# Optimization experiments

Hardware: AMD Instinct MI355X
Metric: run time of the kernel (lower is better)

## Reference

```python
import jax, jax.numpy as jnp
import numpy as np

E = 1024
H = 16
D = E // H
NUM_BUCKETS = 320
MAX_DISTANCE = 800


def _relative_positions_bucket(relative_positions):
    # relative_positions: int32 [T, S]
    num_buckets = NUM_BUCKETS // 2  # 160
    relative_buckets = (relative_positions > 0).astype(jnp.int32) * num_buckets
    rel = jnp.abs(relative_positions)
    max_exact = num_buckets // 2  # 80
    is_small = rel < max_exact
    rel_f = jnp.maximum(rel, 1).astype(jnp.float32)
    large = jnp.log(rel_f / max_exact) / np.log(MAX_DISTANCE / max_exact) * (num_buckets - max_exact)
    large = (max_exact + large).astype(jnp.int32)
    large = jnp.minimum(large, num_buckets - 1)
    relative_buckets = relative_buckets + jnp.where(is_small, rel, large)
    return relative_buckets


def setup_inputs() -> dict:
    key = jax.random.key(0)
    ks = jax.random.split(key, 12)
    B, T = 2, 2048
    s = 0.02
    return {
        "hidden_states": jax.random.normal(ks[0], (B, T, E), dtype=jnp.float32),
        "q_w": jax.random.normal(ks[1], (E, E), dtype=jnp.float32) * s,
        "q_b": jnp.zeros((E,), dtype=jnp.float32),
        "k_w": jax.random.normal(ks[2], (E, E), dtype=jnp.float32) * s,
        "k_b": jnp.zeros((E,), dtype=jnp.float32),
        "v_w": jax.random.normal(ks[3], (E, E), dtype=jnp.float32) * s,
        "v_b": jnp.zeros((E,), dtype=jnp.float32),
        "out_w": jax.random.normal(ks[4], (E, E), dtype=jnp.float32) * s,
        "out_b": jnp.zeros((E,), dtype=jnp.float32),
        "rel_embed": jax.random.normal(ks[5], (NUM_BUCKETS, H), dtype=jnp.float32) * s,
        "gru_const": jnp.ones((1, H, 1, 1), dtype=jnp.float32),
        "gru_w": jax.random.normal(ks[6], (8, D), dtype=jnp.float32) * s,
        "gru_b": jnp.zeros((8,), dtype=jnp.float32),
    }


def reference(hidden_states, q_w, q_b, k_w, k_b, v_w, v_b, out_w, out_b,
              rel_embed, gru_const, gru_w, gru_b):
    B, T, _ = hidden_states.shape
    scaling = D ** (-0.5)

    # --- relative position bias: [H, T, T] ---
    ctx = jnp.arange(T, dtype=jnp.int32)[:, None]
    mem = jnp.arange(T, dtype=jnp.int32)[None, :]
    buckets = _relative_positions_bucket(mem - ctx)          # [T, T]
    position_bias = rel_embed[buckets]                        # [T, T, H]
    position_bias = jnp.transpose(position_bias, (2, 0, 1))   # [H, T, T]

    # --- gate (gru_rel_pos): per (b, h, t) scalar ---
    gated = hidden_states.reshape(B, T, H, D).transpose(0, 2, 1, 3)  # [B,H,T,D]
    proj = jnp.einsum('bhtd,ed->bhte', gated, gru_w) + gru_b         # [B,H,T,8]
    proj = proj.reshape(B, H, T, 2, 4).sum(-1)                        # [B,H,T,2]
    gate = jax.nn.sigmoid(proj)
    gate_a = gate[..., 0:1]
    gate_b = gate[..., 1:2]
    gate_out = gate_a * (gate_b * gru_const - 1.0) + 2.0              # [B,H,T,1]
    gated_position_bias = gate_out * position_bias[None]              # [B,H,T,T]

    # --- attention (same math as F.multi_head_attention_forward eager path) ---
    q = (hidden_states @ q_w.T + q_b).reshape(B, T, H, D).transpose(0, 2, 1, 3) * scaling
    k = (hidden_states @ k_w.T + k_b).reshape(B, T, H, D).transpose(0, 2, 1, 3)
    v = (hidden_states @ v_w.T + v_b).reshape(B, T, H, D).transpose(0, 2, 1, 3)

    scores = jnp.einsum('bhtd,bhsd->bhts', q, k) + gated_position_bias
    attn = jax.nn.softmax(scores, axis=-1)
    ctx_out = jnp.einsum('bhts,bhsd->bhtd', attn, v)                  # [B,H,T,D]
    ctx_out = ctx_out.transpose(0, 2, 1, 3).reshape(B, T, E)
    return ctx_out @ out_w.T + out_b
```

## Files before the change

### kernel.cpp

```cpp
#include <hip/hip_runtime.h>
#include <hip/hip_bf16.h>
#include <math.h>

typedef __bf16 bf16;
typedef __bf16 bf16x4 __attribute__((ext_vector_type(4)));
typedef __bf16 bf16x8 __attribute__((ext_vector_type(8)));
typedef float  f32x4  __attribute__((ext_vector_type(4)));

#define T_SEQ 2048
#define E_DIM 1024
#define H_NUM 16
#define D_DIM 64
#define NDELTA 4095
#define LOG2E 1.4426950408889634f

__device__ __forceinline__ void gld16(const bf16* g, bf16* l) {
  __builtin_amdgcn_global_load_lds((__attribute__((address_space(1))) void*)(g),
                                   (__attribute__((address_space(3))) void*)(l), 16, 0, 0);
}

__global__ void cast_bf16_kernel(const float* __restrict__ src, bf16* __restrict__ dst, int n4) {
  int i = blockIdx.x * blockDim.x + threadIdx.x;
  if (i >= n4) return;
  const float4 v = reinterpret_cast<const float4*>(src)[i];
  bf16x4 o;
  o[0] = (bf16)v.x; o[1] = (bf16)v.y; o[2] = (bf16)v.z; o[3] = (bf16)v.w;
  reinterpret_cast<bf16x4*>(dst)[i] = o;
}

__global__ void cast_w_kernel(const float* __restrict__ q_w, const float* __restrict__ k_w,
                              const float* __restrict__ v_w, const float* __restrict__ o_w,
                              bf16* __restrict__ wcat, bf16* __restrict__ wob) {
  int i = blockIdx.x * 256 + threadIdx.x;
  int sel = blockIdx.y;
  const float* src = (sel == 0) ? q_w : (sel == 1) ? k_w : (sel == 2) ? v_w : o_w;
  bf16* dst = (sel < 3) ? (wcat + (size_t)sel * 1048576) : wob;
  const float4 v = reinterpret_cast<const float4*>(src)[i];
  bf16x4 o;
  o[0] = (bf16)v.x; o[1] = (bf16)v.y; o[2] = (bf16)v.z; o[3] = (bf16)v.w;
  reinterpret_cast<bf16x4*>(dst)[i] = o;
}

__global__ void pb_kernel(const float* __restrict__ rel_embed, float* __restrict__ pbt) {
  int dd = blockIdx.x * 64 + threadIdx.x;
  if (dd >= NDELTA) return;
  int delta = dd - (T_SEQ - 1);
  int bucket = (delta > 0) ? 160 : 0;
  int rel = abs(delta);
  int v;
  if (rel < 80) {
    v = rel;
  } else {
    float rf = (float)(rel < 1 ? 1 : rel);
    float lf = logf(rf / 80.0f) * (80.0f / 2.302585092994046f);
    int lg = 80 + (int)lf;
    v = lg < 159 ? lg : 159;
  }
  bucket += v;
#pragma unroll
  for (int h = 0; h < H_NUM; h++)
    pbt[h * NDELTA + dd] = rel_embed[bucket * H_NUM + h];
}

__global__ __launch_bounds__(256)
void gate_kernel(const float* __restrict__ hs, const float* __restrict__ gru_w,
                 const float* __restrict__ gru_b, const float* __restrict__ gconst,
                 float* __restrict__ gate)
{
  __shared__ float w[512];
  int tid = threadIdx.x;
  w[tid] = gru_w[tid];
  w[tid + 256] = gru_w[tid + 256];
  __syncthreads();
  int idx = blockIdx.x * 256 + tid;
  int h  = idx & 15;
  int bt = idx >> 4;
  const float* x = hs + (size_t)bt * E_DIM + h * D_DIM;
  float acc[8] = {0,0,0,0,0,0,0,0};
  for (int d = 0; d < 64; d += 4) {
    float4 xv = *(const float4*)&x[d];
#pragma unroll
    for (int e = 0; e < 8; e++) {
      acc[e] += xv.x * w[e*64+d] + xv.y * w[e*64+d+1]
              + xv.z * w[e*64+d+2] + xv.w * w[e*64+d+3];
    }
  }
  float p0 = acc[0]+acc[1]+acc[2]+acc[3] + gru_b[0]+gru_b[1]+gru_b[2]+gru_b[3];
  float p1 = acc[4]+acc[5]+acc[6]+acc[7] + gru_b[4]+gru_b[5]+gru_b[6]+gru_b[7];
  float ga = 1.0f / (1.0f + expf(-p0));
  float gb = 1.0f / (1.0f + expf(-p1));
  float g = (ga * (gb * gconst[h] - 1.0f) + 2.0f) * LOG2E;
  int bb = bt >> 11;
  int t  = bt & (T_SEQ - 1);
  gate[((size_t)(bb * H_NUM + h)) * T_SEQ + t] = g;
}

template<int MODE, int N_TOTAL>
__global__ __launch_bounds__(256)
void gemm2_kernel(const bf16* __restrict__ A, const bf16* __restrict__ W,
                  const float* __restrict__ b0, const float* __restrict__ b1,
                  const float* __restrict__ b2, float qalpha,
                  void* __restrict__ out0, void* __restrict__ out1, void* __restrict__ out2)
{
  __shared__ bf16 As[128 * 32];
  __shared__ bf16 Bs[128 * 32];
  const int tid  = threadIdx.x;
  const int lane = tid & 63;
  const int wave = tid >> 6;
  const int m0 = blockIdx.y * 128;
  const int n0 = blockIdx.x * 128;
  const int wm = (wave >> 1) * 64;
  const int wn = (wave & 1) * 64;
  const int qd = lane >> 4;
  const int lm = lane & 15;

  const int row4 = lane >> 2;
  const int col8 = (lane & 3) * 8;
  const bf16* gA0 = A + (size_t)(m0 + wave * 32 + row4) * 1024 + col8;
  const bf16* gA1 = gA0 + (size_t)16 * 1024;
  const bf16* gB0 = W + (size_t)(n0 + wave * 32 + row4) * 1024 + col8;
  const bf16* gB1 = gB0 + (size_t)16 * 1024;
  bf16* lA0 = As + (wave * 2 + 0) * 512;
  bf16* lA1 = As + (wave * 2 + 1) * 512;
  bf16* lB0 = Bs + (wave * 2 + 0) * 512;
  bf16* lB1 = Bs + (wave * 2 + 1) * 512;

  f32x4 acc[4][4] = {};

  for (int k0 = 0; k0 < 1024; k0 += 32) {
    gld16(gA0 + k0, lA0);
    gld16(gA1 + k0, lA1);
    gld16(gB0 + k0, lB0);
    gld16(gB1 + k0, lB1);
    __syncthreads();
    bf16x8 af[4], bfr[4];
#pragma unroll
    for (int i = 0; i < 4; i++) {
      af[i]  = *(const bf16x8*)&As[(wm + i * 16 + lm) * 32 + qd * 8];
      bfr[i] = *(const bf16x8*)&Bs[(wn + i * 16 + lm) * 32 + qd * 8];
    }
#pragma unroll
    for (int im = 0; im < 4; im++)
#pragma unroll
      for (int in = 0; in < 4; in++)
        acc[im][in] = __builtin_amdgcn_mfma_f32_16x16x32_bf16(af[im], bfr[in], acc[im][in], 0, 0, 0);
    __syncthreads();
  }

  const int seg = n0 >> 10;
  const float* bias = (MODE == 0) ? b0 : (seg == 0 ? b0 : (seg == 1 ? b1 : b2));
  const float alpha = (MODE == 1 && seg == 0) ? qalpha : 1.0f;

#pragma unroll
  for (int im = 0; im < 4; im++) {
#pragma unroll
    for (int in = 0; in < 4; in++) {
      const int n  = n0 + wn + in * 16 + lm;
      const int n1 = n & 1023;
      const float bv = bias[n1];
      const int mb = m0 + wm + im * 16 + qd * 4;
      if (MODE == 0) {
        float* o = (float*)out0;
#pragma unroll
        for (int r = 0; r < 4; r++)
          o[(size_t)(mb + r) * 1024 + n1] = acc[im][in][r] + bv;
      } else if (seg == 2) {
        const int bb = mb >> 11;
        const int t  = mb & 2047;
        bf16x4 pk;
#pragma unroll
        for (int r = 0; r < 4; r++) pk[r] = (bf16)(acc[im][in][r] + bv);
        *(bf16x4*)&((bf16*)out2)[((size_t)(bb * 1024 + n1)) * 2048 + t] = pk;
      } else {
        bf16* o = (bf16*)(seg == 0 ? out0 : out1);
#pragma unroll
        for (int r = 0; r < 4; r++)
          o[(size_t)(mb + r) * 1024 + n1] = (bf16)((acc[im][in][r] + bv) * alpha);
      }
    }
  }
}

#define LK 72
__global__ __launch_bounds__(256)
void attn3_kernel(const bf16* __restrict__ Qg, const bf16* __restrict__ Kg,
                  const bf16* __restrict__ Vtg, const float* __restrict__ gate,
                  const float* __restrict__ pbt, bf16* __restrict__ ctx)
{
  __shared__ bf16 Ks[2][64 * LK];
  __shared__ bf16 Vs[2][64 * LK];
  __shared__ bf16 Ps[4][32 * LK];
  __shared__ float pbs[2176];

  const int t0 = blockIdx.x * 128;
  const int h  = blockIdx.y;
  const int b  = blockIdx.z;
  const int tid  = threadIdx.x;
  const int lane = tid & 63;
  const int wave = tid >> 6;
  const int qd = lane >> 4;
  const int lm = lane & 15;

  for (int i = tid; i < 2176; i += 256) {
    int idx = i - t0 + 1920;
    pbs[i] = (idx >= 0 && idx < NDELTA) ? pbt[h * NDELTA + idx] : 0.0f;
  }

  bf16x8 qf[2][2];
  float g[2];
#pragma unroll
  for (int nb = 0; nb < 2; nb++) {
    const int q = t0 + wave * 32 + nb * 16 + lm;
    const bf16* qrow = Qg + (size_t)(b * T_SEQ + q) * E_DIM + h * D_DIM;
    qf[nb][0] = *(const bf16x8*)(qrow + qd * 8);
    qf[nb][1] = *(const bf16x8*)(qrow + 32 + qd * 8);
    g[nb] = gate[((size_t)(b * H_NUM + h)) * T_SEQ + q];
  }

  const int srow = tid >> 2;
  const int scol = (tid & 3) * 16;
  const bf16* kgp = Kg  + ((size_t)(b * T_SEQ) + srow) * E_DIM + h * D_DIM + scol;
  const bf16* vgp = Vtg + ((size_t)(b * 1024) + h * D_DIM + srow) * T_SEQ + scol;

  {
    bf16x8 a0 = *(const bf16x8*)kgp;
    bf16x8 a1 = *(const bf16x8*)(kgp + 8);
    bf16x8 c0 = *(const bf16x8*)vgp;
    bf16x8 c1 = *(const bf16x8*)(vgp + 8);
    *(bf16x8*)&Ks[0][srow * LK + scol]     = a0;
    *(bf16x8*)&Ks[0][srow * LK + scol + 8] = a1;
    *(bf16x8*)&Vs[0][srow * LK + scol]     = c0;
    *(bf16x8*)&Vs[0][srow * LK + scol + 8] = c1;
  }
  __syncthreads();

  f32x4 o[4][2] = {};
  float li[2] = {0.0f, 0.0f};
  bf16* psw = &Ps[wave][0];

  for (int it = 0; it < T_SEQ / 64; it++) {
    const int s0 = it * 64;
    const int buf = it & 1;
    const bool more = (it + 1 < T_SEQ / 64);
    bf16x8 nk0, nk1, nv0, nv1;
    if (more) {
      const bf16* kn = kgp + (size_t)(s0 + 64) * E_DIM;
      const bf16* vn = vgp + (s0 + 64);
      nk0 = *(const bf16x8*)kn; nk1 = *(const bf16x8*)(kn + 8);
      nv0 = *(const bf16x8*)vn; nv1 = *(const bf16x8*)(vn + 8);
    }

    bf16x8 kf[4][2];
#pragma unroll
    for (int mb = 0; mb < 4; mb++) {
      kf[mb][0] = *(const bf16x8*)&Ks[buf][(16 * mb + lm) * LK + qd * 8];
      kf[mb][1] = *(const bf16x8*)&Ks[buf][(16 * mb + lm) * LK + 32 + qd * 8];
    }
#pragma unroll
    for (int nb = 0; nb < 2; nb++) {
      f32x4 sc[4];
#pragma unroll
      for (int mb = 0; mb < 4; mb++) {
        f32x4 t = {};
        t = __builtin_amdgcn_mfma_f32_16x16x32_bf16(kf[mb][0], qf[nb][0], t, 0, 0, 0);
        t = __builtin_amdgcn_mfma_f32_16x16x32_bf16(kf[mb][1], qf[nb][1], t, 0, 0, 0);
        sc[mb] = t;
      }
      const int ib = s0 + 4 * qd + 127 - (wave * 32 + nb * 16 + lm);
      float rs = 0.0f;
#pragma unroll
      for (int mb = 0; mb < 4; mb++) {
        bf16x4 pk;
#pragma unroll
        for (int r = 0; r < 4; r++) {
          float p = __builtin_amdgcn_exp2f(sc[mb][r] + g[nb] * pbs[ib + 16 * mb + r]);
          rs += p;
          pk[r] = (bf16)p;
        }
        *(bf16x4*)&psw[(nb * 16 + lm) * LK + 16 * mb + 4 * qd] = pk;
      }
      li[nb] += rs;
    }
    bf16x8 pf[2][2];
#pragma unroll
    for (int nb = 0; nb < 2; nb++) {
      pf[nb][0] = *(const bf16x8*)&psw[(nb * 16 + lm) * LK + qd * 8];
      pf[nb][1] = *(const bf16x8*)&psw[(nb * 16 + lm) * LK + 32 + qd * 8];
    }
#pragma unroll
    for (int db = 0; db < 4; db++) {
      bf16x8 vf0 = *(const bf16x8*)&Vs[buf][(16 * db + lm) * LK + qd * 8];
      bf16x8 vf1 = *(const bf16x8*)&Vs[buf][(16 * db + lm) * LK + 32 + qd * 8];
#pragma unroll
      for (int nb = 0; nb < 2; nb++) {
        o[db][nb] = __builtin_amdgcn_mfma_f32_16x16x32_bf16(vf0, pf[nb][0], o[db][nb], 0, 0, 0);
        o[db][nb] = __builtin_amdgcn_mfma_f32_16x16x32_bf16(vf1, pf[nb][1], o[db][nb], 0, 0, 0);
      }
    }
    if (more) {
      *(bf16x8*)&Ks[buf ^ 1][srow * LK + scol]     = nk0;
      *(bf16x8*)&Ks[buf ^ 1][srow * LK + scol + 8] = nk1;
      *(bf16x8*)&Vs[buf ^ 1][srow * LK + scol]     = nv0;
      *(bf16x8*)&Vs[buf ^ 1][srow * LK + scol + 8] = nv1;
    }
    __syncthreads();
  }

#pragma unroll
  for (int nb = 0; nb < 2; nb++) {
    li[nb] += __shfl_xor(li[nb], 16);
    li[nb] += __shfl_xor(li[nb], 32);
  }
#pragma unroll
  for (int nb = 0; nb < 2; nb++) {
    const float inv = 1.0f / li[nb];
    const int q = t0 + wave * 32 + nb * 16 + lm;
    bf16* obase = ctx + (size_t)(b * T_SEQ + q) * E_DIM + h * D_DIM + 4 * qd;
#pragma unroll
    for (int db = 0; db < 4; db++) {
      bf16x4 ov;
      ov[0] = (bf16)(o[db][nb][0] * inv); ov[1] = (bf16)(o[db][nb][1] * inv);
      ov[2] = (bf16)(o[db][nb][2] * inv); ov[3] = (bf16)(o[db][nb][3] * inv);
      *(bf16x4*)&obase[16 * db] = ov;
    }
  }
}

extern "C" void kernel_launch(void* const* d_in, const int* in_sizes, int n_in,
                              void* d_out, int out_size, void* d_ws, size_t ws_size,
                              hipStream_t stream)
{
  const float* hs     = (const float*)d_in[0];
  const float* q_w    = (const float*)d_in[1];
  const float* q_b    = (const float*)d_in[2];
  const float* k_w    = (const float*)d_in[3];
  const float* k_b    = (const float*)d_in[4];
  const float* v_w    = (const float*)d_in[5];
  const float* v_b    = (const float*)d_in[6];
  const float* out_w  = (const float*)d_in[7];
  const float* out_b  = (const float*)d_in[8];
  const float* rel    = (const float*)d_in[9];
  const float* gconst = (const float*)d_in[10];
  const float* gru_w  = (const float*)d_in[11];
  const float* gru_b  = (const float*)d_in[12];

  char* p = (char*)d_ws;
  bf16* hsb  = (bf16*)p; p += (size_t)4096 * 1024 * 2;
  bf16* wcat = (bf16*)p; p += (size_t)3072 * 1024 * 2;
  bf16* wob  = (bf16*)p; p += (size_t)1024 * 1024 * 2;
  bf16* Qb   = (bf16*)p; p += (size_t)4096 * 1024 * 2;
  bf16* Kb   = (bf16*)p; p += (size_t)4096 * 1024 * 2;
  bf16* Vtb  = (bf16*)p; p += (size_t)2048 * 2048 * 2;
  bf16* ctxb = (bf16*)p; p += (size_t)4096 * 1024 * 2;
  float* gatep = (float*)p; p += (size_t)2 * H_NUM * T_SEQ * 4;
  float* pbt   = (float*)p; p += (size_t)H_NUM * NDELTA * 4;

  cast_bf16_kernel<<<4096, 256, 0, stream>>>(hs, hsb, 1048576);
  cast_w_kernel<<<dim3(1024, 4), 256, 0, stream>>>(q_w, k_w, v_w, out_w, wcat, wob);
  pb_kernel<<<64, 64, 0, stream>>>(rel, pbt);
  gate_kernel<<<256, 256, 0, stream>>>(hs, gru_w, gru_b, gconst, gatep);

  const float qalpha = 0.125f * LOG2E;
  gemm2_kernel<1, 3072><<<dim3(24, 32), 256, 0, stream>>>(
      hsb, wcat, q_b, k_b, v_b, qalpha, Qb, Kb, Vtb);

  attn3_kernel<<<dim3(T_SEQ / 128, H_NUM, 2), 256, 0, stream>>>(Qb, Kb, Vtb, gatep, pbt, ctxb);

  gemm2_kernel<0, 1024><<<dim3(8, 32), 256, 0, stream>>>(
      ctxb, wob, out_b, nullptr, nullptr, 1.0f, d_out, nullptr, nullptr);
}
```

Before: 227.8 us.

## Double-buffer GEMM loads, shrink output GEMM tile, store position bias as bf16

The GEMM kernel now double-buffers its LDS tiles, issuing the next K-slice's global-to-LDS loads before computing on the current one. It also takes a BM template so the output projection can use 64-row tiles, which doubles its grid to fill more CUs. The attention kernel keeps the position-bias table in LDS as bf16, stored twice with a one-element offset so each lane reads its four bias values with two aligned 2-element loads. This lowers LDS traffic but loses precision in the bias, and the GEMM loop keeps only one sync per iteration, which may leave a race on the buffer being refilled.

```diff
diff --git a/kernel.cpp b/kernel.cpp
--- a/kernel.cpp
+++ b/kernel.cpp
@@ -3,6 +3,7 @@
 #include <math.h>
 
 typedef __bf16 bf16;
+typedef __bf16 bf16x2 __attribute__((ext_vector_type(2)));
 typedef __bf16 bf16x4 __attribute__((ext_vector_type(4)));
 typedef __bf16 bf16x8 __attribute__((ext_vector_type(8)));
 typedef float  f32x4  __attribute__((ext_vector_type(4)));
@@ -95,52 +96,61 @@
   gate[((size_t)(bb * H_NUM + h)) * T_SEQ + t] = g;
 }
 
-template<int MODE, int N_TOTAL>
+template<int MODE, int BM>
 __global__ __launch_bounds__(256)
-void gemm2_kernel(const bf16* __restrict__ A, const bf16* __restrict__ W,
+void gemm3_kernel(const bf16* __restrict__ A, const bf16* __restrict__ W,
                   const float* __restrict__ b0, const float* __restrict__ b1,
                   const float* __restrict__ b2, float qalpha,
                   void* __restrict__ out0, void* __restrict__ out1, void* __restrict__ out2)
 {
-  __shared__ bf16 As[128 * 32];
-  __shared__ bf16 Bs[128 * 32];
+  constexpr int AM = (BM == 128) ? 4 : 2;
+  __shared__ bf16 As[2][BM * 32];
+  __shared__ bf16 Bs[2][128 * 32];
   const int tid  = threadIdx.x;
   const int lane = tid & 63;
   const int wave = tid >> 6;
-  const int m0 = blockIdx.y * 128;
+  const int m0 = blockIdx.y * BM;
   const int n0 = blockIdx.x * 128;
-  const int wm = (wave >> 1) * 64;
+  const int wm = (wave >> 1) * (AM * 16);
   const int wn = (wave & 1) * 64;
   const int qd = lane >> 4;
   const int lm = lane & 15;
 
   const int row4 = lane >> 2;
   const int col8 = (lane & 3) * 8;
-  const bf16* gA0 = A + (size_t)(m0 + wave * 32 + row4) * 1024 + col8;
-  const bf16* gA1 = gA0 + (size_t)16 * 1024;
+  const bf16* gA0 = A + (size_t)(m0 + wave * (BM / 4) + row4) * 1024 + col8;
   const bf16* gB0 = W + (size_t)(n0 + wave * 32 + row4) * 1024 + col8;
   const bf16* gB1 = gB0 + (size_t)16 * 1024;
-  bf16* lA0 = As + (wave * 2 + 0) * 512;
-  bf16* lA1 = As + (wave * 2 + 1) * 512;
-  bf16* lB0 = Bs + (wave * 2 + 0) * 512;
-  bf16* lB1 = Bs + (wave * 2 + 1) * 512;
-
-  f32x4 acc[4][4] = {};
+  bf16* lA = (bf16*)As + wave * (BM / 4) * 32;
+  bf16* lB = (bf16*)Bs + wave * 1024;
+
+  gld16(gA0, lA);
+  if (BM == 128) gld16(gA0 + (size_t)16 * 1024, lA + 512);
+  gld16(gB0, lB);
+  gld16(gB1, lB + 512);
+  __syncthreads();
+
+  f32x4 acc[AM][4] = {};
 
   for (int k0 = 0; k0 < 1024; k0 += 32) {
-    gld16(gA0 + k0, lA0);
-    gld16(gA1 + k0, lA1);
-    gld16(gB0 + k0, lB0);
-    gld16(gB1 + k0, lB1);
-    __syncthreads();
-    bf16x8 af[4], bfr[4];
-#pragma unroll
-    for (int i = 0; i < 4; i++) {
-      af[i]  = *(const bf16x8*)&As[(wm + i * 16 + lm) * 32 + qd * 8];
-      bfr[i] = *(const bf16x8*)&Bs[(wn + i * 16 + lm) * 32 + qd * 8];
-    }
-#pragma unroll
-    for (int im = 0; im < 4; im++)
+    const int buf = (k0 >> 5) & 1;
+    if (k0 + 32 < 1024) {
+      bf16* lA1 = lA + (buf ^ 1) * (BM * 32);
+      bf16* lB1 = lB + (buf ^ 1) * (128 * 32);
+      gld16(gA0 + k0 + 32, lA1);
+      if (BM == 128) gld16(gA0 + (size_t)16 * 1024 + k0 + 32, lA1 + 512);
+      gld16(gB0 + k0 + 32, lB1);
+      gld16(gB1 + k0 + 32, lB1 + 512);
+    }
+    bf16x8 af[AM], bfr[4];
+#pragma unroll
+    for (int i = 0; i < AM; i++)
+      af[i]  = *(const bf16x8*)&As[buf][(wm + i * 16 + lm) * 32 + qd * 8];
+#pragma unroll
+    for (int i = 0; i < 4; i++)
+      bfr[i] = *(const bf16x8*)&Bs[buf][(wn + i * 16 + lm) * 32 + qd * 8];
+#pragma unroll
+    for (int im = 0; im < AM; im++)
 #pragma unroll
       for (int in = 0; in < 4; in++)
         acc[im][in] = __builtin_amdgcn_mfma_f32_16x16x32_bf16(af[im], bfr[in], acc[im][in], 0, 0, 0);
@@ -152,7 +162,7 @@
   const float alpha = (MODE == 1 && seg == 0) ? qalpha : 1.0f;
 
 #pragma unroll
-  for (int im = 0; im < 4; im++) {
+  for (int im = 0; im < AM; im++) {
 #pragma unroll
     for (int in = 0; in < 4; in++) {
       const int n  = n0 + wn + in * 16 + lm;
@@ -182,15 +192,16 @@
 }
 
 #define LK 72
+#define PSK 72
 __global__ __launch_bounds__(256)
-void attn3_kernel(const bf16* __restrict__ Qg, const bf16* __restrict__ Kg,
+void attn5_kernel(const bf16* __restrict__ Qg, const bf16* __restrict__ Kg,
                   const bf16* __restrict__ Vtg, const float* __restrict__ gate,
                   const float* __restrict__ pbt, bf16* __restrict__ ctx)
 {
   __shared__ bf16 Ks[2][64 * LK];
   __shared__ bf16 Vs[2][64 * LK];
-  __shared__ bf16 Ps[4][32 * LK];
-  __shared__ float pbs[2176];
+  __shared__ bf16 Ps[4][32 * PSK];
+  __shared__ bf16 pbs2[2][2184];
 
   const int t0 = blockIdx.x * 128;
   const int h  = blockIdx.y;
@@ -201,9 +212,12 @@
   const int qd = lane >> 4;
   const int lm = lane & 15;
 
-  for (int i = tid; i < 2176; i += 256) {
-    int idx = i - t0 + 1920;
-    pbs[i] = (idx >= 0 && idx < NDELTA) ? pbt[h * NDELTA + idx] : 0.0f;
+  for (int j = tid; j < 2184; j += 256) {
+#pragma unroll
+    for (int c2 = 0; c2 < 2; c2++) {
+      int gidx = j + c2 - 2 - t0 + 1920;
+      pbs2[c2][j] = (bf16)((gidx >= 0 && gidx < NDELTA) ? pbt[h * NDELTA + gidx] : 0.0f);
+    }
   }
 
   bf16x8 qf[2][2];
@@ -216,6 +230,9 @@
     qf[nb][1] = *(const bf16x8*)(qrow + 32 + qd * 8);
     g[nb] = gate[((size_t)(b * H_NUM + h)) * T_SEQ + q];
   }
+
+  const int c = (lm + 1) & 1;
+  const int ebase0 = 4 * qd + 129 - wave * 32 - lm - c;
 
   const int srow = tid >> 2;
   const int scol = (tid & 3) * 16;
@@ -266,26 +283,29 @@
         t = __builtin_amdgcn_mfma_f32_16x16x32_bf16(kf[mb][1], qf[nb][1], t, 0, 0, 0);
         sc[mb] = t;
       }
-      const int ib = s0 + 4 * qd + 127 - (wave * 32 + nb * 16 + lm);
+      const int e0 = ebase0 + s0 - nb * 16;
       float rs = 0.0f;
 #pragma unroll
       for (int mb = 0; mb < 4; mb++) {
+        const bf16x2 bb0 = *(const bf16x2*)&pbs2[c][e0 + 16 * mb];
+        const bf16x2 bb1 = *(const bf16x2*)&pbs2[c][e0 + 16 * mb + 2];
+        const float bias4[4] = {(float)bb0[0], (float)bb0[1], (float)bb1[0], (float)bb1[1]};
         bf16x4 pk;
 #pragma unroll
         for (int r = 0; r < 4; r++) {
-          float p = __builtin_amdgcn_exp2f(sc[mb][r] + g[nb] * pbs[ib + 16 * mb + r]);
+          float p = __builtin_amdgcn_exp2f(sc[mb][r] + g[nb] * bias4[r]);
           rs += p;
           pk[r] = (bf16)p;
         }
-        *(bf16x4*)&psw[(nb * 16 + lm) * LK + 16 * mb + 4 * qd] = pk;
+        *(bf16x4*)&psw[(nb * 16 + lm) * PSK + 16 * mb + 4 * qd] = pk;
       }
       li[nb] += rs;
     }
     bf16x8 pf[2][2];
 #pragma unroll
     for (int nb = 0; nb < 2; nb++) {
-      pf[nb][0] = *(const bf16x8*)&psw[(nb * 16 + lm) * LK + qd * 8];
-      pf[nb][1] = *(const bf16x8*)&psw[(nb * 16 + lm) * LK + 32 + qd * 8];
+      pf[nb][0] = *(const bf16x8*)&psw[(nb * 16 + lm) * PSK + qd * 8];
+      pf[nb][1] = *(const bf16x8*)&psw[(nb * 16 + lm) * PSK + 32 + qd * 8];
     }
 #pragma unroll
     for (int db = 0; db < 4; db++) {
@@ -361,11 +381,11 @@
   gate_kernel<<<256, 256, 0, stream>>>(hs, gru_w, gru_b, gconst, gatep);
 
   const float qalpha = 0.125f * LOG2E;
-  gemm2_kernel<1, 3072><<<dim3(24, 32), 256, 0, stream>>>(
+  gemm3_kernel<1, 128><<<dim3(24, 32), 256, 0, stream>>>(
       hsb, wcat, q_b, k_b, v_b, qalpha, Qb, Kb, Vtb);
 
-  attn3_kernel<<<dim3(T_SEQ / 128, H_NUM, 2), 256, 0, stream>>>(Qb, Kb, Vtb, gatep, pbt, ctxb);
-
-  gemm2_kernel<0, 1024><<<dim3(8, 32), 256, 0, stream>>>(
+  attn5_kernel<<<dim3(T_SEQ / 128, H_NUM, 2), 256, 0, stream>>>(Qb, Kb, Vtb, gatep, pbt, ctxb);
+
+  gemm3_kernel<0, 64><<<dim3(8, 64), 256, 0, stream>>>(
       ctxb, wob, out_b, nullptr, nullptr, 1.0f, d_out, nullptr, nullptr);
 }
```

Result: slower. 258.3 us (+13.4%).
